# Kernel optimization log

Measured on AMD Instinct MI355X. Metric: run time of the kernel, lower is better.

Reference implementation:

```python
import jax, jax.numpy as jnp
import numpy as np

NUM_LAYERS = 3
CHANNELS = 8
IN_CHANNELS = 8
MASK_OUT_STRIDE = 4


def resize_align_corners(x, oh, ow):
    # Bilinear resize with align_corners=True, x: [N, C, H, W]
    n, c, h, w = x.shape
    ys = jnp.linspace(0.0, h - 1.0, oh)
    xs = jnp.linspace(0.0, w - 1.0, ow)
    y0 = jnp.clip(jnp.floor(ys).astype(jnp.int32), 0, h - 2)
    x0 = jnp.clip(jnp.floor(xs).astype(jnp.int32), 0, w - 2)
    wy = (ys - y0.astype(ys.dtype)).astype(x.dtype)[None, None, :, None]
    wx = (xs - x0.astype(xs.dtype)).astype(x.dtype)[None, None, None, :]
    top = x[:, :, y0, :]
    bot = x[:, :, y0 + 1, :]
    row = top * (1.0 - wy) + bot * wy          # [n,c,oh,w]
    left = row[:, :, :, x0]
    right = row[:, :, :, x0 + 1]
    return left * (1.0 - wx) + right * wx       # [n,c,oh,ow]


def aligned_bilinear(t, factor):
    # Faithful port of adet.utils.comm.aligned_bilinear
    if factor == 1:
        return t
    h, w = t.shape[2], t.shape[3]
    t = jnp.pad(t, ((0, 0), (0, 0), (0, 1), (0, 1)), mode="edge")
    oh, ow = factor * h + 1, factor * w + 1
    t = resize_align_corners(t, oh, ow)
    p = factor // 2
    t = jnp.pad(t, ((0, 0), (0, 0), (p, 0), (p, 0)), mode="edge")
    return t[:, :, : oh - 1, : ow - 1]


def reference(mask_feats, mask_head_params, locations_inst, soi, im_inds, fpn_levels, mask_feat_stride):
    N, C, H, W = mask_feats.shape
    n_inst = mask_head_params.shape[0]
    # compute_locations at mask_feat_stride (x fastest, matching torch meshgrid order)
    half = mask_feat_stride // 2
    sx = jnp.arange(W, dtype=mask_feats.dtype) * mask_feat_stride + half
    sy = jnp.arange(H, dtype=mask_feats.dtype) * mask_feat_stride + half
    gy, gx = jnp.meshgrid(sy, sx, indexing="ij")
    locs = jnp.stack([gx.reshape(-1), gy.reshape(-1)], axis=1)  # [HW, 2]
    # relative coords, normalized by size-of-interest of instance's FPN level
    rel = locations_inst[:, None, :] - locs[None, :, :]          # [n, HW, 2]
    rel = jnp.transpose(rel, (0, 2, 1))                          # [n, 2, HW]
    rel = rel / soi[fpn_levels][:, None, None]
    feats = mask_feats[im_inds].reshape(n_inst, IN_CHANNELS, H * W)
    x = jnp.concatenate([rel.astype(mask_feats.dtype), feats], axis=1)  # [n, 10, HW]
    # parse_dynamic_params: split flat params into per-instance weights/biases
    wn = [(IN_CHANNELS + 2) * CHANNELS, CHANNELS * CHANNELS, CHANNELS * 1]
    bn = [CHANNELS, CHANNELS, 1]
    offs = np.cumsum([0] + wn + bn)
    parts = [mask_head_params[:, offs[i]:offs[i + 1]] for i in range(6)]
    w0 = parts[0].reshape(n_inst, CHANNELS, IN_CHANNELS + 2)
    w1 = parts[1].reshape(n_inst, CHANNELS, CHANNELS)
    w2 = parts[2].reshape(n_inst, 1, CHANNELS)
    b0, b1, b2 = parts[3], parts[4], parts[5]
    # per-instance dynamic MLP (1x1 grouped conv == batched matmul)
    x = jax.nn.relu(jnp.einsum("noi,nip->nop", w0, x) + b0[:, :, None])
    x = jax.nn.relu(jnp.einsum("noi,nip->nop", w1, x) + b1[:, :, None])
    x = jnp.einsum("noi,nip->nop", w2, x) + b2[:, :, None]
    logits = x.reshape(n_inst, 1, H, W)
    factor = int(mask_feat_stride // MASK_OUT_STRIDE)
    return aligned_bilinear(logits, factor)


def setup_inputs() -> dict:
    key = jax.random.key(0)
    k0, k1, k2, k3, k4 = jax.random.split(key, 5)
    N, C, H, W = 4, IN_CHANNELS, 128, 192
    n_inst = 128
    stride = 8
    num_gen_params = (IN_CHANNELS + 2) * CHANNELS + CHANNELS * CHANNELS + CHANNELS + CHANNELS + CHANNELS + 1  # 169
    mask_feats = jax.random.normal(k0, (N, C, H, W), dtype=jnp.float32)
    mask_head_params = jax.random.normal(k1, (n_inst, num_gen_params), dtype=jnp.float32) * 0.1
    locations_inst = jax.random.uniform(k2, (n_inst, 2), dtype=jnp.float32) * jnp.array([W * stride, H * stride], jnp.float32)
    soi = jnp.array([64.0, 128.0, 256.0, 512.0, 1024.0], jnp.float32)
    im_inds = jax.random.randint(k3, (n_inst,), 0, N)
    fpn_levels = jax.random.randint(k4, (n_inst,), 0, 5)
    return {
        "mask_feats": mask_feats,
        "mask_head_params": mask_head_params,
        "locations_inst": locations_inst,
        "soi": soi,
        "im_inds": im_inds,
        "fpn_levels": fpn_levels,
        "mask_feat_stride": stride,
    }
```

## Files before the change

### kernel.cpp

```cpp
#include <hip/hip_runtime.h>

#define HH 128
#define WW 192
#define HW (HH * WW)


__device__ __forceinline__ float relu(float v) { return fmaxf(v, 0.0f); }

__global__ __launch_bounds__(512, 4) void dmh_kernel(
    const float* __restrict__ mask_feats,
    const float* __restrict__ params,
    const float* __restrict__ locs,
    const float* __restrict__ soi,
    const int*   __restrict__ im_inds,
    const int*   __restrict__ fpn_levels,
    const int*   __restrict__ stride_p,
    float*       __restrict__ out)
{
    const int tid = threadIdx.x;
    const int c0 = blockIdx.x * 64;
    const int r0 = blockIdx.y * 32;
    const int n  = blockIdx.z;

    __shared__ float sW[176];
    __shared__ float tile[33 * 66];

    if (tid < 169) {
        float v = params[(size_t)n * 169 + tid];
        int d;
        if (tid < 80)       { int o = tid / 10, r = tid - o * 10;
                              d = (r == 0) ? o : (r == 1) ? (8 + o) : (24 + (r - 2) * 8 + o); }
        else if (tid < 144) { int t = tid - 80, o = t >> 3, i = t & 7; d = 88 + i * 8 + o; }
        else if (tid < 152) d = 152 + (tid - 144);
        else if (tid < 160) d = 16 + (tid - 152);
        else if (tid < 168) d = 160 + (tid - 160);
        else                d = 168;
        sW[d] = v;
    }

    const int   stride = *stride_p;
    const float half   = 0.5f * (float)stride;
    const float locx = locs[2 * n + 0];
    const float locy = locs[2 * n + 1];
    const float inv  = 1.0f / soi[fpn_levels[n]];
    const float* fb  = mask_feats + (size_t)im_inds[n] * 8 * HW;

    __syncthreads();

    {
        const int ir = tid >> 4;
        const int ic = (tid & 15) << 2;
        const int rr = r0 + ir, cc = c0 + ic;
        const float* fp = fb + rr * WW + cc;

        float4 xv[8];
        #pragma unroll
        for (int ch = 0; ch < 8; ++ch)
            xv[ch] = *reinterpret_cast<const float4*>(fp + ch * HW);

        const float rxd = -(float)stride * inv;
        float rx[4];
        rx[0] = (locx - (float)(cc * stride) - half) * inv;
        rx[1] = rx[0] + rxd; rx[2] = rx[1] + rxd; rx[3] = rx[2] + rxd;
        const float ry = (locy - (float)(rr * stride) - half) * inv;

        float h[8][4];
        #pragma unroll
        for (int o = 0; o < 8; ++o) {
            float t  = fmaf(sW[8 + o], ry, sW[16 + o]);
            float wx = sW[o];
            #pragma unroll
            for (int j = 0; j < 4; ++j) h[o][j] = fmaf(wx, rx[j], t);
        }
        #pragma unroll
        for (int ch = 0; ch < 8; ++ch) {
            float4 wlo = *reinterpret_cast<const float4*>(&sW[24 + ch * 8]);
            float4 whi = *reinterpret_cast<const float4*>(&sW[28 + ch * 8]);
            float wv[8] = {wlo.x, wlo.y, wlo.z, wlo.w, whi.x, whi.y, whi.z, whi.w};
            float xj[4] = {xv[ch].x, xv[ch].y, xv[ch].z, xv[ch].w};
            #pragma unroll
            for (int o = 0; o < 8; ++o)
                #pragma unroll
                for (int j = 0; j < 4; ++j) h[o][j] = fmaf(wv[o], xj[j], h[o][j]);
        }

        float a[8][4];
        #pragma unroll
        for (int o = 0; o < 8; ++o) {
            float b = sW[160 + o];
            #pragma unroll
            for (int j = 0; j < 4; ++j) a[o][j] = b;
        }
        #pragma unroll
        for (int i = 0; i < 8; ++i) {
            float4 wlo = *reinterpret_cast<const float4*>(&sW[88 + i * 8]);
            float4 whi = *reinterpret_cast<const float4*>(&sW[92 + i * 8]);
            float wv[8] = {wlo.x, wlo.y, wlo.z, wlo.w, whi.x, whi.y, whi.z, whi.w};
            float vj[4] = {relu(h[i][0]), relu(h[i][1]), relu(h[i][2]), relu(h[i][3])};
            #pragma unroll
            for (int o = 0; o < 8; ++o)
                #pragma unroll
                for (int j = 0; j < 4; ++j) a[o][j] = fmaf(wv[o], vj[j], a[o][j]);
        }

        float b2v = sW[168];
        float lg[4] = {b2v, b2v, b2v, b2v};
        #pragma unroll
        for (int o = 0; o < 8; ++o) {
            float w2 = sW[152 + o];
            #pragma unroll
            for (int j = 0; j < 4; ++j) lg[j] = fmaf(w2, relu(a[o][j]), lg[j]);
        }
        #pragma unroll
        for (int j = 0; j < 4; ++j)
            tile[(ir + 1) * 66 + ic + 1 + j] = lg[j];
    }

    if (tid < 97) {
        int r, c;
        if (tid < 65) { r = -1; c = tid - 1; }
        else          { r = tid - 65; c = -1; }
        int rr = min(max(r0 + r, 0), HH - 1);
        int cc = min(max(c0 + c, 0), WW - 1);
        const float* fp = fb + rr * WW + cc;
        float rx  = (locx - (float)(cc * stride) - half) * inv;
        float ry2 = (locy - (float)(rr * stride) - half) * inv;
        float hh[8];
        #pragma unroll
        for (int o = 0; o < 8; ++o)
            hh[o] = fmaf(sW[o], rx, fmaf(sW[8 + o], ry2, sW[16 + o]));
        #pragma unroll
        for (int ch = 0; ch < 8; ++ch) {
            float x = fp[ch * HW];
            #pragma unroll
            for (int o = 0; o < 8; ++o) hh[o] = fmaf(sW[24 + ch * 8 + o], x, hh[o]);
        }
        float aa[8];
        #pragma unroll
        for (int o = 0; o < 8; ++o) aa[o] = sW[160 + o];
        #pragma unroll
        for (int i = 0; i < 8; ++i) {
            float v = relu(hh[i]);
            #pragma unroll
            for (int o = 0; o < 8; ++o) aa[o] = fmaf(sW[88 + i * 8 + o], v, aa[o]);
        }
        float lg = sW[168];
        #pragma unroll
        for (int o = 0; o < 8; ++o) lg = fmaf(sW[152 + o], relu(aa[o]), lg);
        tile[(r + 1) * 66 + (c + 1)] = lg;
    }
    __syncthreads();

    const int kx = tid & 31;
    const int ky = tid >> 5;
    float* ob = out + ((size_t)n * 256 + 2 * r0) * 384 + 2 * c0 + 4 * kx;
    #pragma unroll
    for (int yy = 0; yy < 4; ++yy) {
        int yt = ky * 4 + yy;
        int i  = 2 * r0 + yt - 1;
        int rb = i >> 1;
        int fy = i & 1;
        float wy0 = fy ? 0.5f : 1.0f;
        float wy1 = fy ? 0.5f : 0.0f;
        int lr  = rb - r0 + 1;
        int lr2 = lr + fy;
        const float* ra = &tile[lr  * 66 + 2 * kx];
        const float* rc = &tile[lr2 * 66 + 2 * kx];
        float t0 = fmaf(wy1, rc[0], wy0 * ra[0]);
        float t1 = fmaf(wy1, rc[1], wy0 * ra[1]);
        float t2 = fmaf(wy1, rc[2], wy0 * ra[2]);
        float4 o4;
        o4.x = 0.5f * (t0 + t1);
        o4.y = t1;
        o4.z = 0.5f * (t1 + t2);
        o4.w = t2;
        *reinterpret_cast<float4*>(ob + (size_t)yt * 384) = o4;
    }
}

extern "C" void kernel_launch(void* const* d_in, const int* in_sizes, int n_in,
                              void* d_out, int out_size, void* d_ws, size_t ws_size,
                              hipStream_t stream) {
    const float* mask_feats = (const float*)d_in[0];
    const float* params     = (const float*)d_in[1];
    const float* locs       = (const float*)d_in[2];
    const float* soi        = (const float*)d_in[3];
    const int*   im_inds    = (const int*)d_in[4];
    const int*   fpn_levels = (const int*)d_in[5];
    const int*   stride_p   = (const int*)d_in[6];
    float* out = (float*)d_out;

    dim3 grid(WW / 64, HH / 32, 128);
    dim3 block(512);
    dmh_kernel<<<grid, block, 0, stream>>>(
        mask_feats, params, locs, soi, im_inds, fpn_levels, stride_p, out);
}
```

Measured before the change: 21.10 us.

## Use packed fp16 dot2 for per-pixel MLP and hoist feature loads

Converts the 8x8 weight matrices and per-pixel activations to packed fp16 pairs and computes the three dynamic conv layers with v_dot2 instructions accumulating in fp32, halving the FMA count. Feature loads are issued before the weight-staging barrier so their latency overlaps the parameter setup. Output stores become nontemporal and the launch-bounds occupancy hint is removed. The cost is fp16 rounding of inputs, weights and hidden activations, which may loosen numerical accuracy.

```diff
diff --git a/kernel.cpp b/kernel.cpp
--- a/kernel.cpp
+++ b/kernel.cpp
@@ -4,10 +4,24 @@
 #define WW 192
 #define HW (HH * WW)
 
+typedef float f32x4 __attribute__((ext_vector_type(4)));
+typedef __fp16 h2 __attribute__((ext_vector_type(2)));
 
 __device__ __forceinline__ float relu(float v) { return fmaxf(v, 0.0f); }
 
-__global__ __launch_bounds__(512, 4) void dmh_kernel(
+__device__ __forceinline__ float fdot2(h2 a, h2 b, float c) {
+#if __has_builtin(__builtin_amdgcn_fdot2)
+    return __builtin_amdgcn_fdot2(a, b, c, false);
+#else
+    return fmaf((float)a.x, (float)b.x, fmaf((float)a.y, (float)b.y, c));
+#endif
+}
+__device__ __forceinline__ h2 pkrtz(float a, float b) {
+    return __builtin_amdgcn_cvt_pkrtz(a, b);
+}
+
+
+__global__ __launch_bounds__(512) void dmh_kernel(
     const float* __restrict__ mask_feats,
     const float* __restrict__ params,
     const float* __restrict__ locs,
@@ -22,131 +36,160 @@
     const int r0 = blockIdx.y * 32;
     const int n  = blockIdx.z;
 
-    __shared__ float sW[176];
+    __shared__ h2    sWp[68];
+    __shared__ float sF[33];
     __shared__ float tile[33 * 66];
 
     if (tid < 169) {
         float v = params[(size_t)n * 169 + tid];
-        int d;
-        if (tid < 80)       { int o = tid / 10, r = tid - o * 10;
-                              d = (r == 0) ? o : (r == 1) ? (8 + o) : (24 + (r - 2) * 8 + o); }
-        else if (tid < 144) { int t = tid - 80, o = t >> 3, i = t & 7; d = 88 + i * 8 + o; }
-        else if (tid < 152) d = 152 + (tid - 144);
-        else if (tid < 160) d = 16 + (tid - 152);
-        else if (tid < 168) d = 160 + (tid - 160);
-        else                d = 168;
-        sW[d] = v;
+        __fp16* sWh = reinterpret_cast<__fp16*>(sWp);
+        if (tid < 80) {
+            int o = tid / 10, k = tid - o * 10;
+            if (k == 0)      sF[o] = v;
+            else if (k == 1) sF[8 + o] = v;
+            else { int f = k - 2; sWh[(o * 4 + (f >> 1)) * 2 + (f & 1)] = (__fp16)v; }
+        } else if (tid < 144) {
+            int t = tid - 80, o = t >> 3, i = t & 7;
+            sWh[(32 + o * 4 + (i >> 1)) * 2 + (i & 1)] = (__fp16)v;
+        } else if (tid < 152) {
+            int o = tid - 144;
+            sWh[(64 + (o >> 1)) * 2 + (o & 1)] = (__fp16)v;
+        } else if (tid < 160) sF[16 + (tid - 152)] = v;
+        else if (tid < 168)   sF[24 + (tid - 160)] = v;
+        else                  sF[32] = v;
     }
 
     const int   stride = *stride_p;
-    const float half   = 0.5f * (float)stride;
+    const float half_s = 0.5f * (float)stride;
     const float locx = locs[2 * n + 0];
     const float locy = locs[2 * n + 1];
     const float inv  = 1.0f / soi[fpn_levels[n]];
     const float* fb  = mask_feats + (size_t)im_inds[n] * 8 * HW;
 
+    const int ir = tid >> 4;
+    const int ic = (tid & 15) << 2;
+    const int rr = r0 + ir, cc = c0 + ic;
+    const float* fp = fb + rr * WW + cc;
+
+    f32x4 xv[8];
+    #pragma unroll
+    for (int ch = 0; ch < 8; ++ch)
+        xv[ch] = *reinterpret_cast<const f32x4*>(fp + ch * HW);
+
     __syncthreads();
 
     {
-        const int ir = tid >> 4;
-        const int ic = (tid & 15) << 2;
-        const int rr = r0 + ir, cc = c0 + ic;
-        const float* fp = fb + rr * WW + cc;
-
-        float4 xv[8];
-        #pragma unroll
-        for (int ch = 0; ch < 8; ++ch)
-            xv[ch] = *reinterpret_cast<const float4*>(fp + ch * HW);
-
         const float rxd = -(float)stride * inv;
         float rx[4];
-        rx[0] = (locx - (float)(cc * stride) - half) * inv;
+        rx[0] = (locx - (float)(cc * stride) - half_s) * inv;
         rx[1] = rx[0] + rxd; rx[2] = rx[1] + rxd; rx[3] = rx[2] + rxd;
-        const float ry = (locy - (float)(rr * stride) - half) * inv;
+        const float ry = (locy - (float)(rr * stride) - half_s) * inv;
+
+        h2 xp[4][4];
+        #pragma unroll
+        for (int p = 0; p < 4; ++p)
+            #pragma unroll
+            for (int j = 0; j < 4; ++j)
+                xp[p][j] = pkrtz(xv[2 * p][j], xv[2 * p + 1][j]);
 
         float h[8][4];
         #pragma unroll
         for (int o = 0; o < 8; ++o) {
-            float t  = fmaf(sW[8 + o], ry, sW[16 + o]);
-            float wx = sW[o];
-            #pragma unroll
-            for (int j = 0; j < 4; ++j) h[o][j] = fmaf(wx, rx[j], t);
-        }
-        #pragma unroll
-        for (int ch = 0; ch < 8; ++ch) {
-            float4 wlo = *reinterpret_cast<const float4*>(&sW[24 + ch * 8]);
-            float4 whi = *reinterpret_cast<const float4*>(&sW[28 + ch * 8]);
-            float wv[8] = {wlo.x, wlo.y, wlo.z, wlo.w, whi.x, whi.y, whi.z, whi.w};
-            float xj[4] = {xv[ch].x, xv[ch].y, xv[ch].z, xv[ch].w};
-            #pragma unroll
-            for (int o = 0; o < 8; ++o)
-                #pragma unroll
-                for (int j = 0; j < 4; ++j) h[o][j] = fmaf(wv[o], xj[j], h[o][j]);
-        }
+            const h2 w0 = sWp[o * 4 + 0], w1 = sWp[o * 4 + 1],
+                     w2 = sWp[o * 4 + 2], w3 = sWp[o * 4 + 3];
+            float tO = fmaf(sF[8 + o], ry, sF[16 + o]);
+            float wx = sF[o];
+            #pragma unroll
+            for (int j = 0; j < 4; ++j) {
+                float acc = fmaf(wx, rx[j], tO);
+                acc = fdot2(w0, xp[0][j], acc);
+                acc = fdot2(w1, xp[1][j], acc);
+                acc = fdot2(w2, xp[2][j], acc);
+                acc = fdot2(w3, xp[3][j], acc);
+                h[o][j] = acc;
+            }
+        }
+
+        h2 hp[4][4];
+        #pragma unroll
+        for (int p = 0; p < 4; ++p)
+            #pragma unroll
+            for (int j = 0; j < 4; ++j)
+                hp[p][j] = pkrtz(relu(h[2 * p][j]), relu(h[2 * p + 1][j]));
 
         float a[8][4];
         #pragma unroll
         for (int o = 0; o < 8; ++o) {
-            float b = sW[160 + o];
-            #pragma unroll
-            for (int j = 0; j < 4; ++j) a[o][j] = b;
-        }
-        #pragma unroll
-        for (int i = 0; i < 8; ++i) {
-            float4 wlo = *reinterpret_cast<const float4*>(&sW[88 + i * 8]);
-            float4 whi = *reinterpret_cast<const float4*>(&sW[92 + i * 8]);
-            float wv[8] = {wlo.x, wlo.y, wlo.z, wlo.w, whi.x, whi.y, whi.z, whi.w};
-            float vj[4] = {relu(h[i][0]), relu(h[i][1]), relu(h[i][2]), relu(h[i][3])};
-            #pragma unroll
-            for (int o = 0; o < 8; ++o)
-                #pragma unroll
-                for (int j = 0; j < 4; ++j) a[o][j] = fmaf(wv[o], vj[j], a[o][j]);
-        }
-
-        float b2v = sW[168];
-        float lg[4] = {b2v, b2v, b2v, b2v};
-        #pragma unroll
-        for (int o = 0; o < 8; ++o) {
-            float w2 = sW[152 + o];
-            #pragma unroll
-            for (int j = 0; j < 4; ++j) lg[j] = fmaf(w2, relu(a[o][j]), lg[j]);
-        }
-        #pragma unroll
-        for (int j = 0; j < 4; ++j)
-            tile[(ir + 1) * 66 + ic + 1 + j] = lg[j];
+            const h2 w0 = sWp[32 + o * 4 + 0], w1 = sWp[32 + o * 4 + 1],
+                     w2 = sWp[32 + o * 4 + 2], w3 = sWp[32 + o * 4 + 3];
+            float b1 = sF[24 + o];
+            #pragma unroll
+            for (int j = 0; j < 4; ++j) {
+                float acc = b1;
+                acc = fdot2(w0, hp[0][j], acc);
+                acc = fdot2(w1, hp[1][j], acc);
+                acc = fdot2(w2, hp[2][j], acc);
+                acc = fdot2(w3, hp[3][j], acc);
+                a[o][j] = acc;
+            }
+        }
+
+        const h2 v0 = sWp[64], v1 = sWp[65], v2 = sWp[66], v3 = sWp[67];
+        const float b2v = sF[32];
+        #pragma unroll
+        for (int j = 0; j < 4; ++j) {
+            h2 a0 = pkrtz(relu(a[0][j]), relu(a[1][j]));
+            h2 a1 = pkrtz(relu(a[2][j]), relu(a[3][j]));
+            h2 a2 = pkrtz(relu(a[4][j]), relu(a[5][j]));
+            h2 a3 = pkrtz(relu(a[6][j]), relu(a[7][j]));
+            float lg = b2v;
+            lg = fdot2(v0, a0, lg);
+            lg = fdot2(v1, a1, lg);
+            lg = fdot2(v2, a2, lg);
+            lg = fdot2(v3, a3, lg);
+            tile[(ir + 1) * 66 + ic + 1 + j] = lg;
+        }
     }
 
     if (tid < 97) {
         int r, c;
         if (tid < 65) { r = -1; c = tid - 1; }
         else          { r = tid - 65; c = -1; }
-        int rr = min(max(r0 + r, 0), HH - 1);
-        int cc = min(max(c0 + c, 0), WW - 1);
-        const float* fp = fb + rr * WW + cc;
-        float rx  = (locx - (float)(cc * stride) - half) * inv;
-        float ry2 = (locy - (float)(rr * stride) - half) * inv;
+        int hr = min(max(r0 + r, 0), HH - 1);
+        int hc = min(max(c0 + c, 0), WW - 1);
+        const float* hfp = fb + hr * WW + hc;
+        float rx  = (locx - (float)(hc * stride) - half_s) * inv;
+        float ry2 = (locy - (float)(hr * stride) - half_s) * inv;
+        h2 xp[4];
+        #pragma unroll
+        for (int p = 0; p < 4; ++p)
+            xp[p] = pkrtz(hfp[(2 * p) * HW], hfp[(2 * p + 1) * HW]);
         float hh[8];
         #pragma unroll
-        for (int o = 0; o < 8; ++o)
-            hh[o] = fmaf(sW[o], rx, fmaf(sW[8 + o], ry2, sW[16 + o]));
-        #pragma unroll
-        for (int ch = 0; ch < 8; ++ch) {
-            float x = fp[ch * HW];
-            #pragma unroll
-            for (int o = 0; o < 8; ++o) hh[o] = fmaf(sW[24 + ch * 8 + o], x, hh[o]);
-        }
+        for (int o = 0; o < 8; ++o) {
+            float acc = fmaf(sF[o], rx, fmaf(sF[8 + o], ry2, sF[16 + o]));
+            #pragma unroll
+            for (int p = 0; p < 4; ++p) acc = fdot2(sWp[o * 4 + p], xp[p], acc);
+            hh[o] = acc;
+        }
+        h2 hp[4];
+        #pragma unroll
+        for (int p = 0; p < 4; ++p)
+            hp[p] = pkrtz(relu(hh[2 * p]), relu(hh[2 * p + 1]));
         float aa[8];
         #pragma unroll
-        for (int o = 0; o < 8; ++o) aa[o] = sW[160 + o];
-        #pragma unroll
-        for (int i = 0; i < 8; ++i) {
-            float v = relu(hh[i]);
-            #pragma unroll
-            for (int o = 0; o < 8; ++o) aa[o] = fmaf(sW[88 + i * 8 + o], v, aa[o]);
-        }
-        float lg = sW[168];
-        #pragma unroll
-        for (int o = 0; o < 8; ++o) lg = fmaf(sW[152 + o], relu(aa[o]), lg);
+        for (int o = 0; o < 8; ++o) {
+            float acc = sF[24 + o];
+            #pragma unroll
+            for (int p = 0; p < 4; ++p) acc = fdot2(sWp[32 + o * 4 + p], hp[p], acc);
+            aa[o] = acc;
+        }
+        float lg = sF[32];
+        #pragma unroll
+        for (int p = 0; p < 4; ++p) {
+            h2 ap = pkrtz(relu(aa[2 * p]), relu(aa[2 * p + 1]));
+            lg = fdot2(sWp[64 + p], ap, lg);
+        }
         tile[(r + 1) * 66 + (c + 1)] = lg;
     }
     __syncthreads();
@@ -157,24 +200,24 @@
     #pragma unroll
     for (int yy = 0; yy < 4; ++yy) {
         int yt = ky * 4 + yy;
-        int i  = 2 * r0 + yt - 1;
-        int rb = i >> 1;
-        int fy = i & 1;
+        int iy = yt - 1;
+        int rbl = iy >> 1;
+        int fy = iy & 1;
         float wy0 = fy ? 0.5f : 1.0f;
         float wy1 = fy ? 0.5f : 0.0f;
-        int lr  = rb - r0 + 1;
-        int lr2 = lr + fy;
-        const float* ra = &tile[lr  * 66 + 2 * kx];
-        const float* rc = &tile[lr2 * 66 + 2 * kx];
+        int sr  = rbl + 1;
+        int sr2 = sr + fy;
+        const float* ra = &tile[sr  * 66 + 2 * kx];
+        const float* rc = &tile[sr2 * 66 + 2 * kx];
         float t0 = fmaf(wy1, rc[0], wy0 * ra[0]);
         float t1 = fmaf(wy1, rc[1], wy0 * ra[1]);
         float t2 = fmaf(wy1, rc[2], wy0 * ra[2]);
-        float4 o4;
+        f32x4 o4;
         o4.x = 0.5f * (t0 + t1);
         o4.y = t1;
         o4.z = 0.5f * (t1 + t2);
         o4.w = t2;
-        *reinterpret_cast<float4*>(ob + (size_t)yt * 384) = o4;
+        __builtin_nontemporal_store(o4, reinterpret_cast<f32x4*>(ob + (size_t)yt * 384));
     }
 }
 
```

Result: faster. 20.44 us (-3.1%).
